# Kernel optimization log

Measured on AMD Instinct MI355X. Metric: run time of the kernel, lower is better.

The kernel has to match this reference:

```python
import jax, jax.numpy as jnp
import numpy as np

INPUT_DIM = 1024
HIDDEN_DIM = 2048
NUM_EMB = 4096
EMB_DIM = 256
N = 65536


def setup_inputs() -> dict:
    key = jax.random.key(0)
    ks = jax.random.split(key, 10)
    s = lambda fan_in: 1.0 / np.sqrt(fan_in)
    return {
        "x": jax.random.normal(ks[0], (N, INPUT_DIM), dtype=jnp.float32),
        # encoder: Linear(input_dim, hidden) -> ReLU -> Linear(hidden, emb)
        "W1": jax.random.uniform(ks[1], (INPUT_DIM, HIDDEN_DIM), jnp.float32, -s(INPUT_DIM), s(INPUT_DIM)),
        "b1": jax.random.uniform(ks[2], (HIDDEN_DIM,), jnp.float32, -s(INPUT_DIM), s(INPUT_DIM)),
        "W2": jax.random.uniform(ks[3], (HIDDEN_DIM, EMB_DIM), jnp.float32, -s(HIDDEN_DIM), s(HIDDEN_DIM)),
        "b2": jax.random.uniform(ks[4], (EMB_DIM,), jnp.float32, -s(HIDDEN_DIM), s(HIDDEN_DIM)),
        # codebook (nn.Embedding weight)
        "codebook": jax.random.normal(ks[5], (NUM_EMB, EMB_DIM), dtype=jnp.float32),
        # decoder: Linear(emb, hidden) -> ReLU -> Linear(hidden, input_dim)
        "W3": jax.random.uniform(ks[6], (EMB_DIM, HIDDEN_DIM), jnp.float32, -s(EMB_DIM), s(EMB_DIM)),
        "b3": jax.random.uniform(ks[7], (HIDDEN_DIM,), jnp.float32, -s(EMB_DIM), s(EMB_DIM)),
        "W4": jax.random.uniform(ks[8], (HIDDEN_DIM, INPUT_DIM), jnp.float32, -s(HIDDEN_DIM), s(HIDDEN_DIM)),
        "b4": jax.random.uniform(ks[9], (INPUT_DIM,), jnp.float32, -s(HIDDEN_DIM), s(HIDDEN_DIM)),
    }


def reference(x, W1, b1, W2, b2, codebook, W3, b3, W4, b4):
    # encoder
    h = jax.nn.relu(x @ W1 + b1)
    encoded = h @ W2 + b2                      # [N, E]
    # cdist (squared form; argmin is identical to Euclidean argmin)
    enc_sq = jnp.sum(encoded * encoded, axis=-1, keepdims=True)   # [N, 1]
    cb_sq = jnp.sum(codebook * codebook, axis=-1)                 # [K]
    d2 = enc_sq - 2.0 * (encoded @ codebook.T) + cb_sq            # [N, K]
    indices = jnp.argmin(d2, axis=-1)                             # [N]
    quantized = codebook[indices]                                 # [N, E]
    # decoder
    h2 = jax.nn.relu(quantized @ W3 + b3)
    decoded = h2 @ W4 + b4
    return (quantized, decoded)
```

## Files before the change

### kernel.cpp

```cpp
#include <hip/hip_runtime.h>

#define N_ROWS 65536
#define IN_DIM 1024
#define HID    2048
#define EMB    256
#define NCODE  4096

typedef __attribute__((ext_vector_type(8))) short bf16x8;
typedef __attribute__((ext_vector_type(4))) float f32x4;

__device__ __forceinline__ unsigned short f2bf(float v) {
    unsigned u = __float_as_uint(v);
    u += 0x7FFFu + ((u >> 16) & 1u);
    return (unsigned short)(u >> 16);
}
__device__ __forceinline__ float bf2f(unsigned short h) {
    return __uint_as_float(((unsigned)h) << 16);
}
__device__ __forceinline__ void gload16(const unsigned short* g, unsigned short* l) {
    __builtin_amdgcn_global_load_lds(
        (const __attribute__((address_space(1))) unsigned int*)g,
        (__attribute__((address_space(3))) unsigned int*)l, 16, 0, 0);
}

template<int SPLIT>
__global__ __launch_bounds__(256) void k_conv_w(
    const float* __restrict__ src, unsigned short* __restrict__ dh,
    unsigned short* __restrict__ dl, int NC, int nkt)
{
    const int t = threadIdx.x;
    const int nt = blockIdx.x, kt = blockIdx.y;
    const int kk = t >> 2, j4 = (t & 3) << 2;
    const int k0 = kt << 6, n0 = nt << 4;
    float4 v = *(const float4*)(src + (size_t)(k0 + kk) * NC + n0 + j4);
    size_t tb = ((size_t)nt * nkt + kt) * 1024 + ((kk >> 3) * 128) + (kk & 7);
    float vv[4] = {v.x, v.y, v.z, v.w};
    #pragma unroll
    for (int j = 0; j < 4; ++j) {
        unsigned short h = f2bf(vv[j]);
        dh[tb + (size_t)(j4 + j) * 8] = h;
        if (SPLIT) dl[tb + (size_t)(j4 + j) * 8] = f2bf(vv[j] - bf2f(h));
    }
}

__global__ __launch_bounds__(256) void k_conv_cb(
    const float* __restrict__ cb, unsigned short* __restrict__ ch,
    unsigned short* __restrict__ cl_, float* __restrict__ halfsq)
{
    const int t = threadIdx.x;
    const int ct = blockIdx.x;
    const int cl = t >> 4, f = t & 15;
    const int code = (ct << 4) + cl;
    float ssq = 0.f;
    #pragma unroll
    for (int it = 0; it < 4; ++it) {
        const int k4 = (f << 2) + (it << 6);
        float4 v = *(const float4*)(cb + (size_t)code * EMB + k4);
        ssq += v.x * v.x + v.y * v.y + v.z * v.z + v.w * v.w;
        size_t tb = ((size_t)(ct * 4 + (k4 >> 6))) * 1024 + ((k4 >> 3) & 7) * 128 + cl * 8 + (k4 & 7);
        ushort4 h = { f2bf(v.x), f2bf(v.y), f2bf(v.z), f2bf(v.w) };
        *(ushort4*)&ch[tb] = h;
        ushort4 lo = { f2bf(v.x - bf2f(h.x)), f2bf(v.y - bf2f(h.y)),
                       f2bf(v.z - bf2f(h.z)), f2bf(v.w - bf2f(h.w)) };
        *(ushort4*)&cl_[tb] = lo;
    }
    #pragma unroll
    for (int off = 1; off <= 8; off <<= 1) ssq += __shfl_xor(ssq, off);
    if (f == 0) halfsq[code] = 0.5f * ssq;
}

template<int SPLIT, int AFMT, int OUTT>
__global__ __launch_bounds__(512, 2) void k_layer2(
    const float* __restrict__ A, const unsigned short* __restrict__ At, int a_nkt,
    int lda, int K,
    const unsigned short* __restrict__ Bh, const unsigned short* __restrict__ Bl,
    int b_nkt, const float* __restrict__ bias, int biasoff,
    float* __restrict__ out, unsigned short* __restrict__ outt,
    int outw, int relu, int init, int ny_log2)
{
    constexpr int AL = 8192;
    constexpr int BH = SPLIT ? 16384 : 8192;
    __shared__ __align__(16) unsigned short s_mem[32768];

    const int t = threadIdx.x;
    const int id = blockIdx.x;
    const int m_low = id & 7, rest = id >> 3;
    const int nb = rest & ((1 << ny_log2) - 1);
    const int m0 = (((rest >> ny_log2) << 3) | m_low) * 128;
    const int nb0 = nb * 256;
    const int lane = t & 63, wv = t >> 6;
    const int wm = wv >> 2, wn = wv & 3;
    const int g = lane >> 4, rr = lane & 15;

    f32x4 acc[4][4];
    #pragma unroll
    for (int mi = 0; mi < 4; ++mi)
        #pragma unroll
        for (int ni = 0; ni < 4; ++ni) acc[mi][ni] = (f32x4){0.f, 0.f, 0.f, 0.f};

    for (int kc = 0; kc < K; kc += 64) {
        const int ktile = kc >> 6;
        #pragma unroll
        for (int jj = 0; jj < 2; ++jj) {
            const int j = wv * 2 + jj;
            const size_t gt = ((size_t)(nb0 / 16 + j) * b_nkt + ktile) * 1024;
            #pragma unroll
            for (int half = 0; half < 2; ++half)
                gload16(Bh + gt + half * 512 + lane * 8,
                        &s_mem[BH + j * 1024 + half * 512]);
        }
        if (AFMT == 0) {
            #pragma unroll
            for (int it = 0; it < 4; ++it) {
                int f = t + (it << 9);
                int r = f >> 4, k4 = (f & 15) << 2;
                float4 v = *(const float4*)(A + (size_t)(m0 + r) * lda + kc + k4);
                int mt = r >> 4, rl = r & 15, kb = k4 >> 3, e = k4 & 7;
                int addr = mt * 1024 + kb * 128 + ((rl ^ kb) << 3) + e;
                ushort4 hi, lo;
                hi.x = f2bf(v.x); hi.y = f2bf(v.y); hi.z = f2bf(v.z); hi.w = f2bf(v.w);
                *(ushort4*)&s_mem[addr] = hi;
                if (SPLIT) {
                    lo.x = f2bf(v.x - bf2f(hi.x)); lo.y = f2bf(v.y - bf2f(hi.y));
                    lo.z = f2bf(v.z - bf2f(hi.z)); lo.w = f2bf(v.w - bf2f(hi.w));
                    *(ushort4*)&s_mem[AL + addr] = lo;
                }
            }
        } else {
            const size_t gt = ((size_t)(m0 / 16 + wv) * a_nkt + ktile) * 1024;
            #pragma unroll
            for (int half = 0; half < 2; ++half)
                gload16(At + gt + half * 512 + lane * 8,
                        &s_mem[wv * 1024 + half * 512]);
        }
        __syncthreads();
        __builtin_amdgcn_s_setprio(1);
        #pragma unroll
        for (int s = 0; s < 2; ++s) {
            const int kb = (s << 2) + g;
            bf16x8 a_h[4], a_l[4], b_h[4], b_l[4];
            #pragma unroll
            for (int i = 0; i < 4; ++i) {
                int arow = (AFMT == 0) ? (((rr ^ kb) & 15) << 3) : (rr << 3);
                int aaddr = (wm * 4 + i) * 1024 + kb * 128 + arow;
                a_h[i] = *(const bf16x8*)&s_mem[aaddr];
                if (SPLIT) a_l[i] = *(const bf16x8*)&s_mem[AL + aaddr];
                int baddr = (wn * 4 + i) * 1024 + kb * 128 + (rr << 3);
                b_h[i] = *(const bf16x8*)&s_mem[BH + baddr];
                if (SPLIT)
                    b_l[i] = *(const bf16x8*)(Bl +
                        ((size_t)(nb0 / 16 + wn * 4 + i) * b_nkt + ktile) * 1024
                        + kb * 128 + (rr << 3));
            }
            #pragma unroll
            for (int mi = 0; mi < 4; ++mi)
                #pragma unroll
                for (int ni = 0; ni < 4; ++ni) {
                    acc[mi][ni] = __builtin_amdgcn_mfma_f32_16x16x32_bf16(a_h[mi], b_h[ni], acc[mi][ni], 0, 0, 0);
                    if (SPLIT) {
                        acc[mi][ni] = __builtin_amdgcn_mfma_f32_16x16x32_bf16(a_l[mi], b_h[ni], acc[mi][ni], 0, 0, 0);
                        acc[mi][ni] = __builtin_amdgcn_mfma_f32_16x16x32_bf16(a_h[mi], b_l[ni], acc[mi][ni], 0, 0, 0);
                    }
                }
        }
        __builtin_amdgcn_s_setprio(0);
        __syncthreads();
    }

    if (OUTT == 0) {
        float* sf = (float*)s_mem;
        for (int rm = 0; rm < 2; ++rm) {
            if (wm == rm) {
                #pragma unroll
                for (int mi = 0; mi < 4; ++mi)
                    #pragma unroll
                    for (int ni = 0; ni < 4; ++ni)
                        #pragma unroll
                        for (int rg = 0; rg < 4; ++rg)
                            sf[(mi * 16 + g * 4 + rg) * 256 + wn * 64 + ni * 16 + rr] = acc[mi][ni][rg];
            }
            __syncthreads();
            #pragma unroll
            for (int it = 0; it < 8; ++it) {
                int f = t + (it << 9);
                int r = f >> 6, c4 = (f & 63) << 2;
                float4 v = *(const float4*)&sf[r * 256 + c4];
                int gr = m0 + rm * 64 + r, gc = nb0 + c4;
                float* op = out + (size_t)gr * outw + gc;
                if (init) {
                    v.x += bias[biasoff + gc + 0]; v.y += bias[biasoff + gc + 1];
                    v.z += bias[biasoff + gc + 2]; v.w += bias[biasoff + gc + 3];
                } else {
                    float4 o = *(const float4*)op;
                    v.x += o.x; v.y += o.y; v.z += o.z; v.w += o.w;
                }
                if (relu) {
                    v.x = fmaxf(v.x, 0.f); v.y = fmaxf(v.y, 0.f);
                    v.z = fmaxf(v.z, 0.f); v.w = fmaxf(v.w, 0.f);
                }
                *(float4*)op = v;
            }
            __syncthreads();
        }
    } else {
        #pragma unroll
        for (int mi = 0; mi < 4; ++mi)
            #pragma unroll
            for (int ni = 0; ni < 4; ++ni) {
                const int c = wn * 64 + ni * 16 + rr;
                float bb = bias[biasoff + nb0 + c];
                #pragma unroll
                for (int rg = 0; rg < 4; ++rg) {
                    float v = acc[mi][ni][rg] + bb;
                    if (relu) v = fmaxf(v, 0.f);
                    int addr = ((wm * 4 + mi) * 4 + wn) * 1024
                             + (ni * 2 + (rr >> 3)) * 128 + (g * 4 + rg) * 8 + (rr & 7);
                    s_mem[addr] = f2bf(v);
                }
            }
        __syncthreads();
        #pragma unroll
        for (int it = 0; it < 8; ++it) {
            int f = t + (it << 9);
            int tl = f >> 7, w8 = f & 127;
            size_t gaddr = ((size_t)(m0 / 16 + (tl >> 2)) * outw + nb0 / 64 + (tl & 3)) * 1024;
            *(float4*)(outt + gaddr + w8 * 8) = *(const float4*)&s_mem[tl * 1024 + w8 * 8];
        }
    }
}

__global__ __launch_bounds__(512, 2) void k_dist(
    float* encq, const unsigned short* __restrict__ ch,
    const unsigned short* __restrict__ cl,
    const float* __restrict__ hsq, const float* __restrict__ cb)
{
    __shared__ __align__(16) unsigned short s_cb[2][16384];
    __shared__ int s_c1[256], s_c2[256];

    const int t = threadIdx.x;
    const int lane = t & 63, wv = t >> 6;
    const int g = lane >> 4, rr = lane & 15;
    const int r0 = blockIdx.x * 256;

    bf16x8 eh[2][8], el[2][8];
    #pragma unroll
    for (int rg = 0; rg < 2; ++rg) {
        const float* ep = encq + (size_t)(r0 + wv * 32 + rg * 16 + rr) * EMB + g * 8;
        #pragma unroll
        for (int s = 0; s < 8; ++s) {
            float4 v0 = *(const float4*)(ep + s * 32);
            float4 v1 = *(const float4*)(ep + s * 32 + 4);
            float vv[8] = {v0.x, v0.y, v0.z, v0.w, v1.x, v1.y, v1.z, v1.w};
            bf16x8 a, b;
            #pragma unroll
            for (int j = 0; j < 8; ++j) {
                unsigned short h = f2bf(vv[j]);
                a[j] = (short)h;
                b[j] = (short)f2bf(vv[j] - bf2f(h));
            }
            eh[rg][s] = a; el[rg][s] = b;
        }
    }
    float b1v[2][4], b2v[2][4]; int i1v[2][4], i2v[2][4];
    #pragma unroll
    for (int rg = 0; rg < 2; ++rg)
        #pragma unroll
        for (int r2 = 0; r2 < 4; ++r2) {
            b1v[rg][r2] = -1e30f; b2v[rg][r2] = -1e30f;
            i1v[rg][r2] = 0; i2v[rg][r2] = 0;
        }

    #define STAGE(buf, c)                                                              \
        {                                                                              \
            const unsigned short* gh_ = ch + (size_t)(c) * 8192 + wv * 1024;           \
            const unsigned short* gl_ = cl + (size_t)(c) * 8192 + wv * 1024;           \
            _Pragma("unroll")                                                          \
            for (int i_ = 0; i_ < 2; ++i_) {                                           \
                gload16(gh_ + i_ * 512 + lane * 8, &s_cb[buf][wv * 1024 + i_ * 512]);  \
                gload16(gl_ + i_ * 512 + lane * 8, &s_cb[buf][8192 + wv * 1024 + i_ * 512]); \
            }                                                                          \
        }

    #define COMPUTE(cur, c, hv_)                                                       \
        {                                                                              \
            f32x4 ahh[2][2], ahl[2][2], alh[2][2];                                     \
            _Pragma("unroll")                                                          \
            for (int rg = 0; rg < 2; ++rg)                                             \
                _Pragma("unroll")                                                      \
                for (int ci = 0; ci < 2; ++ci) {                                       \
                    ahh[rg][ci] = (f32x4){0.f, 0.f, 0.f, 0.f};                         \
                    ahl[rg][ci] = (f32x4){0.f, 0.f, 0.f, 0.f};                         \
                    alh[rg][ci] = (f32x4){0.f, 0.f, 0.f, 0.f};                         \
                }                                                                      \
            __builtin_amdgcn_s_setprio(1);                                             \
            _Pragma("unroll")                                                          \
            for (int s = 0; s < 8; ++s) {                                              \
                const int ktile = s >> 1, kb = ((s & 1) << 2) + g;                     \
                _Pragma("unroll")                                                      \
                for (int ci = 0; ci < 2; ++ci) {                                       \
                    const int off = (ci * 4 + ktile) * 1024 + kb * 128 + rr * 8;       \
                    bf16x8 bh = *(const bf16x8*)&s_cb[cur][off];                       \
                    bf16x8 bl = *(const bf16x8*)&s_cb[cur][8192 + off];                \
                    _Pragma("unroll")                                                  \
                    for (int rg = 0; rg < 2; ++rg) {                                   \
                        ahh[rg][ci] = __builtin_amdgcn_mfma_f32_16x16x32_bf16(eh[rg][s], bh, ahh[rg][ci], 0, 0, 0); \
                        ahl[rg][ci] = __builtin_amdgcn_mfma_f32_16x16x32_bf16(eh[rg][s], bl, ahl[rg][ci], 0, 0, 0); \
                        alh[rg][ci] = __builtin_amdgcn_mfma_f32_16x16x32_bf16(el[rg][s], bh, alh[rg][ci], 0, 0, 0); \
                    }                                                                  \
                }                                                                      \
            }                                                                          \
            __builtin_amdgcn_s_setprio(0);                                             \
            _Pragma("unroll")                                                          \
            for (int rg = 0; rg < 2; ++rg)                                             \
                _Pragma("unroll")                                                      \
                for (int ci = 0; ci < 2; ++ci) {                                       \
                    f32x4 av = ahh[rg][ci] + ahl[rg][ci] + alh[rg][ci];                \
                    const int code = ((c) << 5) + (ci << 4) + rr;                      \
                    const float hs = __shfl(hv_, ci * 16 + rr);                        \
                    _Pragma("unroll")                                                  \
                    for (int r2 = 0; r2 < 4; ++r2) {                                   \
                        float v = av[r2] - hs;                                         \
                        bool bt1 = (v > b1v[rg][r2]) || (v == b1v[rg][r2] && code < i1v[rg][r2]); \
                        bool bt2 = (v > b2v[rg][r2]) || (v == b2v[rg][r2] && code < i2v[rg][r2]); \
                        if (bt1) { b2v[rg][r2] = b1v[rg][r2]; i2v[rg][r2] = i1v[rg][r2]; \
                                   b1v[rg][r2] = v; i1v[rg][r2] = code; }              \
                        else if (bt2) { b2v[rg][r2] = v; i2v[rg][r2] = code; }         \
                    }                                                                  \
                }                                                                      \
        }

    STAGE(0, 0)
    int cur = 0;
    for (int c = 0; c < 127; ++c) {
        STAGE(cur ^ 1, c + 1)
        float hv_ = hsq[(c << 5) + (lane & 31)];
        asm volatile("s_waitcnt vmcnt(5)" ::: "memory");
        __builtin_amdgcn_s_barrier();
        __builtin_amdgcn_sched_barrier(0);
        COMPUTE(cur, c, hv_)
        asm volatile("" ::: "memory");
        __builtin_amdgcn_s_barrier();
        cur ^= 1;
    }
    {
        float hv_ = hsq[(127 << 5) + (lane & 31)];
        asm volatile("s_waitcnt vmcnt(0)" ::: "memory");
        __builtin_amdgcn_s_barrier();
        __builtin_amdgcn_sched_barrier(0);
        COMPUTE(cur, 127, hv_)
    }
    #undef STAGE
    #undef COMPUTE

    #pragma unroll
    for (int off = 1; off <= 8; off <<= 1) {
        #pragma unroll
        for (int rg = 0; rg < 2; ++rg)
            #pragma unroll
            for (int r2 = 0; r2 < 4; ++r2) {
                float ob1 = __shfl_xor(b1v[rg][r2], off), ob2 = __shfl_xor(b2v[rg][r2], off);
                int oi1 = __shfl_xor(i1v[rg][r2], off), oi2 = __shfl_xor(i2v[rg][r2], off);
                bool ofirst = (ob1 > b1v[rg][r2]) || (ob1 == b1v[rg][r2] && oi1 < i1v[rg][r2]);
                if (ofirst) {
                    bool mysec = (b1v[rg][r2] > ob2) || (b1v[rg][r2] == ob2 && i1v[rg][r2] < oi2);
                    b2v[rg][r2] = mysec ? b1v[rg][r2] : ob2; i2v[rg][r2] = mysec ? i1v[rg][r2] : oi2;
                    b1v[rg][r2] = ob1; i1v[rg][r2] = oi1;
                } else {
                    bool osec = (ob1 > b2v[rg][r2]) || (ob1 == b2v[rg][r2] && oi1 < i2v[rg][r2]);
                    b2v[rg][r2] = osec ? ob1 : b2v[rg][r2]; i2v[rg][r2] = osec ? oi1 : i2v[rg][r2];
                }
            }
    }
    if (rr == 0) {
        #pragma unroll
        for (int rg = 0; rg < 2; ++rg)
            #pragma unroll
            for (int r2 = 0; r2 < 4; ++r2) {
                int rl = wv * 32 + rg * 16 + g * 4 + r2;
                s_c1[rl] = i1v[rg][r2]; s_c2[rl] = i2v[rg][r2];
            }
    }
    __syncthreads();

    for (int rloc = 0; rloc < 32; ++rloc) {
        const int row = wv * 32 + rloc;
        const int c1 = s_c1[row], c2 = s_c2[row];
        float4 ev = *(const float4*)(encq + (size_t)(r0 + row) * EMB + lane * 4);
        float4 v1 = *(const float4*)(cb + (size_t)c1 * EMB + lane * 4);
        float4 v2 = *(const float4*)(cb + (size_t)c2 * EMB + lane * 4);
        float d1 = ev.x * v1.x + ev.y * v1.y + ev.z * v1.z + ev.w * v1.w;
        float d2 = ev.x * v2.x + ev.y * v2.y + ev.z * v2.z + ev.w * v2.w;
        #pragma unroll
        for (int off = 1; off <= 32; off <<= 1) {
            d1 += __shfl_xor(d1, off);
            d2 += __shfl_xor(d2, off);
        }
        if (lane == 0) {
            float s1 = d1 - hsq[c1], s2 = d2 - hsq[c2];
            bool keep1 = (s1 > s2) || (s1 == s2 && c1 < c2);
            s_c1[row] = keep1 ? c1 : c2;
        }
    }
    __syncthreads();
    #pragma unroll
    for (int it = 0; it < 32; ++it) {
        int f = t + (it << 9);
        int row = f >> 6, c4 = (f & 63) << 2;
        int bi = s_c1[row];
        *(float4*)(encq + (size_t)(r0 + row) * EMB + c4) =
            *(const float4*)(cb + (size_t)bi * EMB + c4);
    }
}

__global__ __launch_bounds__(256) void k_dec_fb(
    const float* __restrict__ qz,
    const float* __restrict__ W3, const float* __restrict__ b3,
    const float* __restrict__ W4, const float* __restrict__ b4,
    float* __restrict__ outd) {
    __shared__ float s_q[8][EMB];
    __shared__ float s_h2[8][HID];
    const int t = threadIdx.x;
    const int row0 = blockIdx.x * 8;
    #pragma unroll
    for (int r = 0; r < 8; ++r) s_q[r][t] = qz[(size_t)(row0 + r) * EMB + t];
    __syncthreads();
    for (int gg = 0; gg < 8; ++gg) {
        const int j = (gg << 8) + t;
        float acc[8];
        #pragma unroll
        for (int r = 0; r < 8; ++r) acc[r] = 0.f;
        const float* wp = W3 + j;
        for (int e = 0; e < EMB; e += 4) {
            const float w0 = wp[(size_t)(e + 0) * HID];
            const float w1v = wp[(size_t)(e + 1) * HID];
            const float w2v = wp[(size_t)(e + 2) * HID];
            const float w3v = wp[(size_t)(e + 3) * HID];
            #pragma unroll
            for (int r = 0; r < 8; ++r) {
                const float4 qv = *reinterpret_cast<const float4*>(&s_q[r][e]);
                acc[r] = fmaf(qv.x, w0, acc[r]);
                acc[r] = fmaf(qv.y, w1v, acc[r]);
                acc[r] = fmaf(qv.z, w2v, acc[r]);
                acc[r] = fmaf(qv.w, w3v, acc[r]);
            }
        }
        const float bb = b3[j];
        #pragma unroll
        for (int r = 0; r < 8; ++r) s_h2[r][j] = fmaxf(acc[r] + bb, 0.f);
    }
    __syncthreads();
    float acc4[8][4];
    #pragma unroll
    for (int r = 0; r < 8; ++r)
        #pragma unroll
        for (int ci = 0; ci < 4; ++ci) acc4[r][ci] = 0.f;
    const float* w4p = W4 + t;
    for (int k = 0; k < HID; k += 4) {
        float wv[4][4];
        #pragma unroll
        for (int ki = 0; ki < 4; ++ki)
            #pragma unroll
            for (int ci = 0; ci < 4; ++ci)
                wv[ki][ci] = w4p[(size_t)(k + ki) * IN_DIM + (ci << 8)];
        #pragma unroll
        for (int r = 0; r < 8; ++r) {
            const float4 hv = *reinterpret_cast<const float4*>(&s_h2[r][k]);
            #pragma unroll
            for (int ci = 0; ci < 4; ++ci) {
                acc4[r][ci] = fmaf(hv.x, wv[0][ci], acc4[r][ci]);
                acc4[r][ci] = fmaf(hv.y, wv[1][ci], acc4[r][ci]);
                acc4[r][ci] = fmaf(hv.z, wv[2][ci], acc4[r][ci]);
                acc4[r][ci] = fmaf(hv.w, wv[3][ci], acc4[r][ci]);
            }
        }
    }
    #pragma unroll
    for (int ci = 0; ci < 4; ++ci) {
        const float bb = b4[(ci << 8) + t];
        #pragma unroll
        for (int r = 0; r < 8; ++r)
            outd[(size_t)(row0 + r) * IN_DIM + (ci << 8) + t] = acc4[r][ci] + bb;
    }
}

extern "C" void kernel_launch(void* const* d_in, const int* in_sizes, int n_in,
                              void* d_out, int out_size, void* d_ws, size_t ws_size,
                              hipStream_t stream) {
    const float* x  = (const float*)d_in[0];
    const float* W1 = (const float*)d_in[1];
    const float* b1 = (const float*)d_in[2];
    const float* W2 = (const float*)d_in[3];
    const float* b2 = (const float*)d_in[4];
    const float* cb = (const float*)d_in[5];
    const float* W3 = (const float*)d_in[6];
    const float* b3 = (const float*)d_in[7];
    const float* W4 = (const float*)d_in[8];
    const float* b4 = (const float*)d_in[9];

    float* outq = (float*)d_out;
    float* outd = outq + (size_t)N_ROWS * EMB;

    unsigned short* ou = (unsigned short*)outd;
    unsigned short* W1Th = ou;
    unsigned short* W1Tl = ou + 2097152;
    unsigned short* W2Th = ou + 4194304;
    unsigned short* W2Tl = ou + 4718592;
    unsigned short* cbh  = ou + 5242880;
    unsigned short* cbl  = ou + 6291456;
    float* halfsq = outd + 3670016;
    float* hbuf   = outd + 4194304;
    float* enc    = outq;

    const bool fastdec = ws_size >= (size_t)72351744;
    unsigned short* W3Th = (unsigned short*)d_ws;
    unsigned short* W4Th = W3Th + 524288;
    unsigned short* h2t  = (unsigned short*)((char*)d_ws + 5242880);

    k_conv_w<1><<<dim3(128, 16), 256, 0, stream>>>(W1, W1Th, W1Tl, HID, 16);
    k_conv_w<1><<<dim3(16, 32), 256, 0, stream>>>(W2, W2Th, W2Tl, EMB, 32);
    k_conv_cb<<<256, 256, 0, stream>>>(cb, cbh, cbl, halfsq);
    if (fastdec) {
        k_conv_w<0><<<dim3(128, 4), 256, 0, stream>>>(W3, W3Th, nullptr, HID, 4);
        k_conv_w<0><<<dim3(64, 32), 256, 0, stream>>>(W4, W4Th, nullptr, IN_DIM, 32);
    }
    for (int q = 0; q < 4; ++q) {
        k_layer2<1, 0, 0><<<1024, 512, 0, stream>>>(
            x, nullptr, 0, IN_DIM, IN_DIM,
            W1Th + (size_t)q * 524288, W1Tl + (size_t)q * 524288, 16,
            b1, q * 512, hbuf, nullptr, 512, 1, 1, 1);
        k_layer2<1, 0, 0><<<512, 512, 0, stream>>>(
            hbuf, nullptr, 0, 512, 512,
            W2Th + (size_t)q * 8192, W2Tl + (size_t)q * 8192, 32,
            b2, 0, enc, nullptr, EMB, 0, q == 0, 0);
    }
    k_dist<<<256, 512, 0, stream>>>(enc, cbh, cbl, halfsq, cb);
    if (fastdec) {
        for (int s = 0; s < 4; ++s) {
            const size_t roff = (size_t)s * 16384;
            k_layer2<0, 0, 1><<<1024, 512, 0, stream>>>(
                outq + roff * EMB, nullptr, 0, EMB, EMB,
                W3Th, nullptr, 4,
                b3, 0, nullptr, h2t, 32, 1, 0, 3);
            k_layer2<0, 1, 0><<<512, 512, 0, stream>>>(
                nullptr, h2t, 32, 0, HID,
                W4Th, nullptr, 32,
                b4, 0, outd + roff * IN_DIM, nullptr, IN_DIM, 0, 1, 2);
        }
    } else {
        k_dec_fb<<<N_ROWS / 8, 256, 0, stream>>>(outq, W3, b3, W4, b4, outd);
    }
}
```

Before: 2.452 ms.

## Store encoder hidden as pre-tiled bf16 hi/lo pairs and pre-tile quantized input

The first encoder layer now writes its ReLU hidden activations directly as tiled bf16 hi and lo halves instead of fp32. The second layer loads both halves asynchronously with global-to-LDS loads rather than converting fp32 in-kernel. For the decoder, the quantized codes are converted once into a tiled bf16 layout so the first decoder GEMM can use the async-load path. This removes per-tile fp32 reads and conversions on the A side. The cost is an extra store pass in the epilogue and one extra conversion kernel.

After: 2.436 ms. About the same (-0.7%).

```diff
diff --git a/kernel.cpp b/kernel.cpp
--- a/kernel.cpp
+++ b/kernel.cpp
@@ -43,6 +43,18 @@
     }
 }
 
+__global__ __launch_bounds__(256) void k_conv_a(
+    const float* __restrict__ src, unsigned short* __restrict__ dst, int Kw, int nkt)
+{
+    const int t = threadIdx.x;
+    const int mt = blockIdx.x, kt = blockIdx.y;
+    const int rr = t >> 4, k4 = (t & 15) << 2;
+    float4 v = *(const float4*)(src + (size_t)(mt * 16 + rr) * Kw + kt * 64 + k4);
+    size_t addr = ((size_t)mt * nkt + kt) * 1024 + (k4 >> 3) * 128 + rr * 8 + (k4 & 7);
+    ushort4 h = { f2bf(v.x), f2bf(v.y), f2bf(v.z), f2bf(v.w) };
+    *(ushort4*)&dst[addr] = h;
+}
+
 __global__ __launch_bounds__(256) void k_conv_cb(
     const float* __restrict__ cb, unsigned short* __restrict__ ch,
     unsigned short* __restrict__ cl_, float* __restrict__ halfsq)
@@ -71,11 +83,13 @@
 
 template<int SPLIT, int AFMT, int OUTT>
 __global__ __launch_bounds__(512, 2) void k_layer2(
-    const float* __restrict__ A, const unsigned short* __restrict__ At, int a_nkt,
+    const float* __restrict__ A, const unsigned short* __restrict__ At,
+    const unsigned short* __restrict__ Atl, int a_nkt,
     int lda, int K,
     const unsigned short* __restrict__ Bh, const unsigned short* __restrict__ Bl,
     int b_nkt, const float* __restrict__ bias, int biasoff,
     float* __restrict__ out, unsigned short* __restrict__ outt,
+    unsigned short* __restrict__ outt2,
     int outw, int relu, int init, int ny_log2)
 {
     constexpr int AL = 8192;
@@ -132,6 +146,12 @@
             for (int half = 0; half < 2; ++half)
                 gload16(At + gt + half * 512 + lane * 8,
                         &s_mem[wv * 1024 + half * 512]);
+            if (AFMT == 2) {
+                #pragma unroll
+                for (int half = 0; half < 2; ++half)
+                    gload16(Atl + gt + half * 512 + lane * 8,
+                            &s_mem[AL + wv * 1024 + half * 512]);
+            }
         }
         __syncthreads();
         __builtin_amdgcn_s_setprio(1);
@@ -203,28 +223,35 @@
             __syncthreads();
         }
     } else {
-        #pragma unroll
-        for (int mi = 0; mi < 4; ++mi)
-            #pragma unroll
-            for (int ni = 0; ni < 4; ++ni) {
-                const int c = wn * 64 + ni * 16 + rr;
-                float bb = bias[biasoff + nb0 + c];
+        const int npass = (OUTT == 2) ? 2 : 1;
+        for (int pass = 0; pass < npass; ++pass) {
+            #pragma unroll
+            for (int mi = 0; mi < 4; ++mi)
                 #pragma unroll
-                for (int rg = 0; rg < 4; ++rg) {
-                    float v = acc[mi][ni][rg] + bb;
-                    if (relu) v = fmaxf(v, 0.f);
-                    int addr = ((wm * 4 + mi) * 4 + wn) * 1024
-                             + (ni * 2 + (rr >> 3)) * 128 + (g * 4 + rg) * 8 + (rr & 7);
-                    s_mem[addr] = f2bf(v);
+                for (int ni = 0; ni < 4; ++ni) {
+                    const int c = wn * 64 + ni * 16 + rr;
+                    float bb = bias[biasoff + nb0 + c];
+                    #pragma unroll
+                    for (int rg = 0; rg < 4; ++rg) {
+                        float v = acc[mi][ni][rg] + bb;
+                        if (relu) v = fmaxf(v, 0.f);
+                        unsigned short hi = f2bf(v);
+                        unsigned short w = (pass == 0) ? hi : f2bf(v - bf2f(hi));
+                        int addr = ((wm * 4 + mi) * 4 + wn) * 1024
+                                 + (ni * 2 + (rr >> 3)) * 128 + (g * 4 + rg) * 8 + (rr & 7);
+                        s_mem[addr] = w;
+                    }
                 }
-            }
-        __syncthreads();
-        #pragma unroll
-        for (int it = 0; it < 8; ++it) {
-            int f = t + (it << 9);
-            int tl = f >> 7, w8 = f & 127;
-            size_t gaddr = ((size_t)(m0 / 16 + (tl >> 2)) * outw + nb0 / 64 + (tl & 3)) * 1024;
-            *(float4*)(outt + gaddr + w8 * 8) = *(const float4*)&s_mem[tl * 1024 + w8 * 8];
+            __syncthreads();
+            unsigned short* dst = (pass == 0) ? outt : outt2;
+            #pragma unroll
+            for (int it = 0; it < 8; ++it) {
+                int f = t + (it << 9);
+                int tl = f >> 7, w8 = f & 127;
+                size_t gaddr = ((size_t)(m0 / 16 + (tl >> 2)) * outw + nb0 / 64 + (tl & 3)) * 1024;
+                *(float4*)(dst + gaddr + w8 * 8) = *(const float4*)&s_mem[tl * 1024 + w8 * 8];
+            }
+            __syncthreads();
         }
     }
 }
@@ -508,8 +535,10 @@
     unsigned short* cbh  = ou + 5242880;
     unsigned short* cbl  = ou + 6291456;
     float* halfsq = outd + 3670016;
-    float* hbuf   = outd + 4194304;
-    float* enc    = outq;
+    unsigned short* h_hi = (unsigned short*)(outd + 4194304);
+    unsigned short* h_lo = h_hi + 33554432;
+    unsigned short* qt = (unsigned short*)(outd + 58720256);
+    float* enc = outq;
 
     const bool fastdec = ws_size >= (size_t)72351744;
     unsigned short* W3Th = (unsigned short*)d_ws;
@@ -524,27 +553,28 @@
         k_conv_w<0><<<dim3(64, 32), 256, 0, stream>>>(W4, W4Th, nullptr, IN_DIM, 32);
     }
     for (int q = 0; q < 4; ++q) {
-        k_layer2<1, 0, 0><<<1024, 512, 0, stream>>>(
-            x, nullptr, 0, IN_DIM, IN_DIM,
+        k_layer2<1, 0, 2><<<1024, 512, 0, stream>>>(
+            x, nullptr, nullptr, 0, IN_DIM, IN_DIM,
             W1Th + (size_t)q * 524288, W1Tl + (size_t)q * 524288, 16,
-            b1, q * 512, hbuf, nullptr, 512, 1, 1, 1);
-        k_layer2<1, 0, 0><<<512, 512, 0, stream>>>(
-            hbuf, nullptr, 0, 512, 512,
+            b1, q * 512, nullptr, h_hi, h_lo, 8, 1, 0, 1);
+        k_layer2<1, 2, 0><<<512, 512, 0, stream>>>(
+            nullptr, h_hi, h_lo, 8, 0, 512,
             W2Th + (size_t)q * 8192, W2Tl + (size_t)q * 8192, 32,
-            b2, 0, enc, nullptr, EMB, 0, q == 0, 0);
+            b2, 0, enc, nullptr, nullptr, EMB, 0, q == 0, 0);
     }
     k_dist<<<256, 512, 0, stream>>>(enc, cbh, cbl, halfsq, cb);
     if (fastdec) {
+        k_conv_a<<<dim3(4096, 4), 256, 0, stream>>>(outq, qt, EMB, 4);
         for (int s = 0; s < 4; ++s) {
             const size_t roff = (size_t)s * 16384;
-            k_layer2<0, 0, 1><<<1024, 512, 0, stream>>>(
-                outq + roff * EMB, nullptr, 0, EMB, EMB,
+            k_layer2<0, 1, 1><<<1024, 512, 0, stream>>>(
+                nullptr, qt + (size_t)s * 4194304, nullptr, 4, 0, EMB,
                 W3Th, nullptr, 4,
-                b3, 0, nullptr, h2t, 32, 1, 0, 3);
+                b3, 0, nullptr, h2t, nullptr, 32, 1, 0, 3);
             k_layer2<0, 1, 0><<<512, 512, 0, stream>>>(
-                nullptr, h2t, 32, 0, HID,
+                nullptr, h2t, nullptr, 32, 0, HID,
                 W4Th, nullptr, 32,
-                b4, 0, outd + roff * IN_DIM, nullptr, IN_DIM, 0, 1, 2);
+                b4, 0, outd + roff * IN_DIM, nullptr, nullptr, IN_DIM, 0, 1, 2);
         }
     } else {
         k_dec_fb<<<N_ROWS / 8, 256, 0, stream>>>(outq, W3, b3, W4, b4, outd);
```
